# Optimization experiments

Hardware: AMD Instinct MI355X
Metric: run time of the kernel (lower is better)

Reference implementation:

```python
import jax, jax.numpy as jnp
import numpy as np

N_NODES = 100000
N_EDGES = 1600000
NUM_GRAPHS = 64
D = 128      # num_node_features
H = 256      # hidden_dim
OUT = 1      # output_dim
GA = 6       # num_graph_attributes


def setup_inputs() -> dict:
    key = jax.random.key(0)
    ks = jax.random.split(key, 20)
    p = lambda k, shape: (jax.random.normal(k, shape, jnp.float32) * 0.02)
    return {
        "x": jax.random.normal(ks[0], (N_NODES, D), jnp.float32),
        "edge_index": jax.random.randint(ks[1], (2, N_EDGES), 0, N_NODES),
        "batch": jnp.sort(jax.random.randint(ks[2], (N_NODES,), 0, NUM_GRAPHS)),
        "graph_attr": jax.random.normal(ks[3], (NUM_GRAPHS, GA), jnp.float32),
        # conv1 MLP: Linear(D->H), ReLU, Linear(H->H)
        "w1a": p(ks[4], (D, H)), "b1a": p(ks[5], (H,)),
        "w1b": p(ks[6], (H, H)), "b1b": p(ks[7], (H,)),
        # conv2 MLP: Linear(H->H), ReLU, Linear(H->H)
        "w2a": p(ks[8], (H, H)), "b2a": p(ks[9], (H,)),
        "w2b": p(ks[10], (H, H)), "b2b": p(ks[11], (H,)),
        # head
        "wf1": p(ks[12], (H + GA, H)), "bf1": p(ks[13], (H,)),
        "wf2": p(ks[14], (H, OUT)), "bf2": p(ks[15], (OUT,)),
    }


def _gin_conv(x, src, dst, wa, ba, wb, bb):
    # GINConv with default eps=0: MLP((1+0)*x_i + sum_{j->i} x_j)
    agg = jax.ops.segment_sum(x[src], dst, num_segments=N_NODES)  # [N, d]
    h = x + agg
    h = jax.nn.relu(h @ wa + ba)
    return h @ wb + bb


def reference(x, edge_index, batch, graph_attr,
              w1a, b1a, w1b, b1b, w2a, b2a, w2b, b2b,
              wf1, bf1, wf2, bf2):
    src, dst = edge_index[0], edge_index[1]
    h = jax.nn.relu(_gin_conv(x, src, dst, w1a, b1a, w1b, b1b))  # [N, H]
    h = _gin_conv(h, src, dst, w2a, b2a, w2b, b2b)               # [N, H]
    # global mean pool per graph
    sums = jax.ops.segment_sum(h, batch, num_segments=NUM_GRAPHS)          # [G, H]
    cnts = jax.ops.segment_sum(jnp.ones((h.shape[0], 1), h.dtype), batch,
                               num_segments=NUM_GRAPHS)                    # [G, 1]
    pooled = sums / jnp.maximum(cnts, 1.0)
    g = jnp.concatenate([pooled, graph_attr.reshape(-1, GA)], axis=1)      # [G, H+GA]
    g = jax.nn.relu(g @ wf1 + bf1)
    return g @ wf2 + bf2                                                   # [G, OUT]
```

## Files before the change

kernel.cpp:

```cpp
#include <hip/hip_runtime.h>

#define N_NODES 100000
#define N_EDGES 1600000
#define NGRAPH  64
#define DIN     128
#define HID     256
#define GA      6

#define NBUCK  98
#define BSHIFT 10
#define BCAP   20480

typedef __attribute__((ext_vector_type(8))) short bf16x8;
typedef __attribute__((ext_vector_type(4))) float f32x4;

__device__ __forceinline__ unsigned short f2bf(float f) {
  unsigned int u = __float_as_uint(f);
  u += 0x7fffu + ((u >> 16) & 1u);
  return (unsigned short)(u >> 16);
}
__device__ __forceinline__ float bf_lo(unsigned int u) { return __uint_as_float(u << 16); }
__device__ __forceinline__ float bf_hi(unsigned int u) { return __uint_as_float(u & 0xffff0000u); }
__device__ __forceinline__ unsigned int packbf(float lo, float hi) {
  return (unsigned int)f2bf(lo) | ((unsigned int)f2bf(hi) << 16);
}

__device__ __forceinline__ void gload16(const void* g, void* l) {
  __builtin_amdgcn_global_load_lds(
      (const __attribute__((address_space(1))) unsigned int*)g,
      (__attribute__((address_space(3))) unsigned int*)l, 16, 0, 0);
}


__global__ __launch_bounds__(256) void cvt_x_kernel(const float* __restrict__ in,
                                                    unsigned short* __restrict__ out) {
  size_t idx = ((size_t)blockIdx.x * 256 + threadIdx.x) * 4;
  float4 v = *(const float4*)&in[idx];
  ushort4 o;
  o.x = f2bf(v.x); o.y = f2bf(v.y); o.z = f2bf(v.z); o.w = f2bf(v.w);
  *(ushort4*)&out[idx] = o;
}

__global__ __launch_bounds__(256) void cvt_w_all(const float* __restrict__ w1a,
                                                 const float* __restrict__ w1b,
                                                 const float* __restrict__ w2a,
                                                 const float* __restrict__ w2b,
                                                 unsigned short* __restrict__ o1a,
                                                 unsigned short* __restrict__ o1b,
                                                 unsigned short* __restrict__ o2a,
                                                 unsigned short* __restrict__ o2b) {
  int bid = blockIdx.x, tid = threadIdx.x;
  const float* in; unsigned short* out; int shift, idx;
  if (bid < 128)      { in = w1a; out = o1a; shift = 7; idx = bid * 256 + tid; }
  else if (bid < 384) { in = w1b; out = o1b; shift = 8; idx = (bid - 128) * 256 + tid; }
  else if (bid < 640) { in = w2a; out = o2a; shift = 8; idx = (bid - 384) * 256 + tid; }
  else                { in = w2b; out = o2b; shift = 8; idx = (bid - 640) * 256 + tid; }
  int K = 1 << shift;
  int n = idx >> shift;
  int k = idx & (K - 1);
  out[idx] = f2bf(in[(size_t)k * HID + n]);
}


__global__ __launch_bounds__(256) void bin_kernel(const int* __restrict__ esrc,
                                                  const int* __restrict__ edst,
                                                  int* __restrict__ cursor,
                                                  unsigned int* __restrict__ tmp) {
  __shared__ unsigned int pk[4096];
  __shared__ int hist[NBUCK], lbase[NBUCK + 1], gbase[NBUCK], lcur[NBUCK];
  const int tid = threadIdx.x;
  const int lane = tid & 63;
  const int ebase = blockIdx.x * 4096;
  const int n = min(4096, N_EDGES - ebase);
  if (tid < NBUCK) hist[tid] = 0;
  __syncthreads();
  unsigned int pkv[16]; int bk[16];
#pragma unroll
  for (int i = 0; i < 16; i++) {
    int e = ebase + i * 256 + tid;
    bk[i] = -1;
    if (e < N_EDGES) {
      int s = esrc[e], d = edst[e];
      bk[i] = d >> BSHIFT;
      pkv[i] = (unsigned int)s | ((unsigned int)(d & ((1 << BSHIFT) - 1)) << 17);
      atomicAdd(&hist[bk[i]], 1);
    }
  }
  __syncthreads();
  if (tid < 64) {
    int i0 = 2 * tid, i1 = i0 + 1;
    int a0 = (i0 < NBUCK) ? hist[i0] : 0;
    int a1 = (i1 < NBUCK) ? hist[i1] : 0;
    int p = a0 + a1, sc = p;
#pragma unroll
    for (int off = 1; off < 64; off <<= 1) {
      int t = __shfl_up(sc, off);
      if (lane >= off) sc += t;
    }
    int excl = sc - p;
    if (i0 < NBUCK) lbase[i0] = excl;
    if (i1 < NBUCK) lbase[i1] = excl + a0;
    if (tid == 63) lbase[NBUCK] = sc;
  }
  __syncthreads();
  if (tid < NBUCK) {
    int c = hist[tid];
    gbase[tid] = c ? atomicAdd(&cursor[tid], c) : 0;
    lcur[tid] = lbase[tid];
  }
  __syncthreads();
#pragma unroll
  for (int i = 0; i < 16; i++) {
    if (bk[i] >= 0) {
      int pos = atomicAdd(&lcur[bk[i]], 1);
      pk[pos] = pkv[i];
    }
  }
  __syncthreads();
#pragma unroll
  for (int i = 0; i < 16; i++) {
    int idx = i * 256 + tid;
    if (idx < n) {
      int lo = 0, hi = NBUCK;
      while (hi - lo > 1) {
        int mid = (lo + hi) >> 1;
        if (lbase[mid] <= idx) lo = mid; else hi = mid;
      }
      tmp[(size_t)lo * BCAP + gbase[lo] + (idx - lbase[lo])] = pk[idx];
    }
  }
}


__global__ __launch_bounds__(512) void sort_kernel(const unsigned int* __restrict__ tmp,
                                                   const int* __restrict__ cnt,
                                                   int* __restrict__ csr,
                                                   int* __restrict__ ssrc) {
  __shared__ int nhist[1024], ncur[1024];
  __shared__ int bb[NBUCK];
  __shared__ int wsum[8];
  const int b = blockIdx.x;
  const int tid = threadIdx.x;
  const int lane = tid & 63, wid = tid >> 6;
  if (tid < 64) {
    int i0 = 2 * tid, i1 = i0 + 1;
    int a0 = (i0 < NBUCK) ? cnt[i0] : 0;
    int a1 = (i1 < NBUCK) ? cnt[i1] : 0;
    int p = a0 + a1, sc = p;
#pragma unroll
    for (int off = 1; off < 64; off <<= 1) {
      int t = __shfl_up(sc, off);
      if (lane >= off) sc += t;
    }
    int excl = sc - p;
    if (i0 < NBUCK) bb[i0] = excl;
    if (i1 < NBUCK) bb[i1] = excl + a0;
  }
  nhist[tid] = 0; nhist[tid + 512] = 0;
  __syncthreads();
  const int myCnt = cnt[b];
  const int ebase = bb[b];
  const unsigned int* srcp = tmp + (size_t)b * BCAP;
  for (int i = tid; i < myCnt; i += 512)
    atomicAdd(&nhist[srcp[i] >> 17], 1);
  __syncthreads();
  int i0 = 2 * tid;
  int a0 = nhist[i0], a1 = nhist[i0 + 1];
  int p = a0 + a1, sc = p;
#pragma unroll
  for (int off = 1; off < 64; off <<= 1) {
    int t = __shfl_up(sc, off);
    if (lane >= off) sc += t;
  }
  if (lane == 63) wsum[wid] = sc;
  __syncthreads();
  if (tid < 8) {
    int ws = wsum[tid];
#pragma unroll
    for (int off = 1; off < 8; off <<= 1) {
      int t = __shfl_up(ws, off);
      if (tid >= off) ws += t;
    }
    wsum[tid] = ws;
  }
  __syncthreads();
  int excl = ((wid > 0) ? wsum[wid - 1] : 0) + sc - p;
  ncur[i0] = excl;
  ncur[i0 + 1] = excl + a0;
  int node0 = (b << BSHIFT) + i0;
  if (node0 < N_NODES) csr[node0] = ebase + excl;
  if (node0 + 1 < N_NODES) csr[node0 + 1] = ebase + excl + a0;
  if (b == 0 && tid == 0) csr[N_NODES] = N_EDGES;
  __syncthreads();
  for (int i = tid; i < myCnt; i += 512) {
    unsigned int pe = srcp[i];
    int pos = atomicAdd(&ncur[pe >> 17], 1);
    ssrc[ebase + pos] = (int)(pe & 0x1FFFF);
  }
}


__global__ __launch_bounds__(256) void agg1_kernel(const unsigned int* __restrict__ x,
                                                   const int* __restrict__ csr,
                                                   const int* __restrict__ ssrc,
                                                   unsigned int* __restrict__ out) {
  int node = blockIdx.x * 4 + (threadIdx.x >> 6);
  int lane = threadIdx.x & 63;
  unsigned int u = x[(size_t)node * 64 + lane];
  float alo = bf_lo(u), ahi = bf_hi(u);
  int s = csr[node], e = csr[node + 1];
  int i = s;
  for (; i + 4 <= e; i += 4) {
    int n0 = ssrc[i], n1 = ssrc[i + 1], n2 = ssrc[i + 2], n3 = ssrc[i + 3];
    unsigned int v0 = x[(size_t)n0 * 64 + lane];
    unsigned int v1 = x[(size_t)n1 * 64 + lane];
    unsigned int v2 = x[(size_t)n2 * 64 + lane];
    unsigned int v3 = x[(size_t)n3 * 64 + lane];
    alo += bf_lo(v0) + bf_lo(v1) + bf_lo(v2) + bf_lo(v3);
    ahi += bf_hi(v0) + bf_hi(v1) + bf_hi(v2) + bf_hi(v3);
  }
  for (; i < e; i++) {
    unsigned int v = x[(size_t)ssrc[i] * 64 + lane];
    alo += bf_lo(v); ahi += bf_hi(v);
  }
  out[(size_t)node * 64 + lane] = packbf(alo, ahi);
}

__global__ __launch_bounds__(256) void agg2_kernel(const uint2* __restrict__ x,
                                                   const int* __restrict__ csr,
                                                   const int* __restrict__ ssrc,
                                                   uint2* __restrict__ out) {
  int node = blockIdx.x * 4 + (threadIdx.x >> 6);
  int lane = threadIdx.x & 63;
  uint2 u = x[(size_t)node * 64 + lane];
  float a0 = bf_lo(u.x), a1 = bf_hi(u.x), a2 = bf_lo(u.y), a3 = bf_hi(u.y);
  int s = csr[node], e = csr[node + 1];
  int i = s;
  for (; i + 4 <= e; i += 4) {
    int n0 = ssrc[i], n1 = ssrc[i + 1], n2 = ssrc[i + 2], n3 = ssrc[i + 3];
    uint2 v0 = x[(size_t)n0 * 64 + lane];
    uint2 v1 = x[(size_t)n1 * 64 + lane];
    uint2 v2 = x[(size_t)n2 * 64 + lane];
    uint2 v3 = x[(size_t)n3 * 64 + lane];
    a0 += bf_lo(v0.x) + bf_lo(v1.x) + bf_lo(v2.x) + bf_lo(v3.x);
    a1 += bf_hi(v0.x) + bf_hi(v1.x) + bf_hi(v2.x) + bf_hi(v3.x);
    a2 += bf_lo(v0.y) + bf_lo(v1.y) + bf_lo(v2.y) + bf_lo(v3.y);
    a3 += bf_hi(v0.y) + bf_hi(v1.y) + bf_hi(v2.y) + bf_hi(v3.y);
  }
  for (; i < e; i++) {
    uint2 v = x[(size_t)ssrc[i] * 64 + lane];
    a0 += bf_lo(v.x); a1 += bf_hi(v.x);
    a2 += bf_lo(v.y); a3 += bf_hi(v.y);
  }
  uint2 o;
  o.x = packbf(a0, a1);
  o.y = packbf(a2, a3);
  out[(size_t)node * 64 + lane] = o;
}

template<int K1, bool RELU2>
__global__ __launch_bounds__(512, 1)
void mlp_fused(const unsigned short* __restrict__ A,
               const unsigned short* __restrict__ W1t,
               const float* __restrict__ b1,
               const unsigned short* __restrict__ W2t,
               const float* __restrict__ b2,
               unsigned short* __restrict__ C) {
  __shared__ unsigned short Hsl[128 * 256];
  __shared__ unsigned short Wsl[2][256 * 64];
  unsigned short* const Ab0 = Hsl;
  unsigned short* const Ab1 = Hsl + 128 * 64;

  const int tid = threadIdx.x;
  const int lane = tid & 63;
  const int w = tid >> 6;
  const int wm = w >> 2;
  const int wn = w & 3;
  const int l15 = lane & 15, l4 = lane >> 4;
  const int l7 = l15 & 7;
  const int rowBase = blockIdx.x * 128;
  constexpr int S1 = K1 / 64;

  auto stageW = [&](const unsigned short* Wt, int K, int k0, unsigned short* dst) {
#pragma unroll
    for (int i = 0; i < 4; i++) {
      int c = i * 512 + tid;
      int n = c >> 3, koL = c & 7;
      int koS = koL ^ (n & 7);
      gload16(&Wt[(size_t)n * K + k0 + koS * 8], dst + (size_t)c * 8);
    }
  };
  auto stageA = [&](int k0, unsigned short* dst) {
#pragma unroll
    for (int i = 0; i < 2; i++) {
      int c = i * 512 + tid;
      int m = c >> 3, koL = c & 7;
      int koS = koL ^ (m & 7);
      int gr = rowBase + m; if (gr >= N_NODES) gr = N_NODES - 1;
      gload16(&A[(size_t)gr * K1 + k0 + koS * 8], dst + (size_t)c * 8);
    }
  };

  stageA(0, Ab0);
  stageW(W1t, K1, 0, Wsl[0]);
  __syncthreads();

  f32x4 acc[4][4] = {};

  for (int s = 0; s < S1; s++) {
    if (s + 1 < S1) {
      stageA((s + 1) * 64, ((s + 1) & 1) ? Ab1 : Ab0);
      stageW(W1t, K1, (s + 1) * 64, Wsl[(s + 1) & 1]);
    } else {
      stageW(W2t, 256, 0, Wsl[(s + 1) & 1]);
    }
    const unsigned short* Ac = (s & 1) ? Ab1 : Ab0;
    const unsigned short* Wc = Wsl[s & 1];
#pragma unroll
    for (int kk = 0; kk < 2; kk++) {
      int koX = (kk * 4 + l4) ^ l7;
      bf16x8 a[4], b[4];
#pragma unroll
      for (int f = 0; f < 4; f++) {
        int rowA = wm * 64 + f * 16 + l15;
        int rowB = wn * 64 + f * 16 + l15;
        a[f] = *(const bf16x8*)&Ac[(size_t)(rowA * 64 + koX * 8)];
        b[f] = *(const bf16x8*)&Wc[(size_t)(rowB * 64 + koX * 8)];
      }
#pragma unroll
      for (int fm = 0; fm < 4; fm++)
#pragma unroll
        for (int fn = 0; fn < 4; fn++)
          acc[fm][fn] = __builtin_amdgcn_mfma_f32_16x16x32_bf16(a[fm], b[fn], acc[fm][fn], 0, 0, 0);
    }
    __syncthreads();
  }

#pragma unroll
  for (int fm = 0; fm < 4; fm++) {
#pragma unroll
    for (int fn = 0; fn < 4; fn++) {
      int col = wn * 64 + fn * 16 + l15;
      float bb = b1[col];
#pragma unroll
      for (int j = 0; j < 4; j++) {
        int m = wm * 64 + fm * 16 + l4 * 4 + j;
        float v = fmaxf(acc[fm][fn][j] + bb, 0.f);
        float pv = __shfl_xor(v, 1);
        if ((l15 & 1) == 0) {
          int idx = m * 256 + (((col >> 3) ^ (m & 7)) << 3) + (col & 7);
          *(unsigned int*)&Hsl[idx] = packbf(v, pv);
        }
      }
      acc[fm][fn] = (f32x4){0.f, 0.f, 0.f, 0.f};
    }
  }
  __syncthreads();

  int wp = S1 & 1;
  for (int s2 = 0; s2 < 4; s2++) {
    if (s2 < 3) stageW(W2t, 256, (s2 + 1) * 64, Wsl[wp ^ 1]);
    const unsigned short* Wc = Wsl[wp];
#pragma unroll
    for (int kk = 0; kk < 2; kk++) {
      int ko = kk * 4 + l4;
      int koXw = ko ^ l7;
      int koXh = (s2 * 8 + ko) ^ l7;
      bf16x8 a[4], b[4];
#pragma unroll
      for (int f = 0; f < 4; f++) {
        int rowA = wm * 64 + f * 16 + l15;
        int rowB = wn * 64 + f * 16 + l15;
        a[f] = *(const bf16x8*)&Hsl[(size_t)(rowA * 256 + koXh * 8)];
        b[f] = *(const bf16x8*)&Wc[(size_t)(rowB * 64 + koXw * 8)];
      }
#pragma unroll
      for (int fm = 0; fm < 4; fm++)
#pragma unroll
        for (int fn = 0; fn < 4; fn++)
          acc[fm][fn] = __builtin_amdgcn_mfma_f32_16x16x32_bf16(a[fm], b[fn], acc[fm][fn], 0, 0, 0);
    }
    __syncthreads();
    wp ^= 1;
  }

#pragma unroll
  for (int fm = 0; fm < 4; fm++) {
    int r0 = rowBase + wm * 64 + fm * 16 + l4 * 4;
#pragma unroll
    for (int fn = 0; fn < 4; fn++) {
      int col = wn * 64 + fn * 16 + l15;
      float bb = b2[col];
#pragma unroll
      for (int j = 0; j < 4; j++) {
        int r = r0 + j;
        if (r < N_NODES) {
          float v = acc[fm][fn][j] + bb;
          if (RELU2) v = fmaxf(v, 0.f);
          C[(size_t)r * HID + col] = f2bf(v);
        }
      }
    }
  }
}


__global__ __launch_bounds__(256) void pool_kernel(const unsigned short* __restrict__ H,
                                                   const int* __restrict__ batch,
                                                   float* __restrict__ sums,
                                                   float* __restrict__ cnts) {
  int d = threadIdx.x;
  int n0 = blockIdx.x * 128;
  int n1 = n0 + 128; if (n1 > N_NODES) n1 = N_NODES;
  int cur = batch[n0];
  float run = 0.f, runc = 0.f;
  for (int i = n0; i < n1; i++) {
    int b = batch[i];
    if (b != cur) {
      atomicAdd(&sums[(size_t)cur * HID + d], run);
      if (d == 0) atomicAdd(&cnts[cur], runc);
      run = 0.f; runc = 0.f; cur = b;
    }
    run += __uint_as_float(((unsigned int)H[(size_t)i * HID + d]) << 16);
    runc += 1.f;
  }
  atomicAdd(&sums[(size_t)cur * HID + d], run);
  if (d == 0) atomicAdd(&cnts[cur], runc);
}


__global__ __launch_bounds__(256) void head_kernel(const float* __restrict__ sums,
                                                   const float* __restrict__ cnts,
                                                   const float* __restrict__ gattr,
                                                   const float* __restrict__ wf1,
                                                   const float* __restrict__ bf1,
                                                   const float* __restrict__ wf2,
                                                   const float* __restrict__ bf2,
                                                   float* __restrict__ out) {
  int g = blockIdx.x, tid = threadIdx.x;
  __shared__ float gv[HID + GA];
  __shared__ float red[256];
  float c = cnts[g]; c = fmaxf(c, 1.0f);
  gv[tid] = sums[(size_t)g * HID + tid] / c;
  if (tid < GA) gv[HID + tid] = gattr[g * GA + tid];
  __syncthreads();
  float acc = bf1[tid];
  for (int k = 0; k < HID + GA; k++)
    acc = fmaf(gv[k], wf1[(size_t)k * HID + tid], acc);
  float h = fmaxf(acc, 0.f);
  red[tid] = h * wf2[tid];
  __syncthreads();
  for (int s = 128; s > 0; s >>= 1) {
    if (tid < s) red[tid] += red[tid + s];
    __syncthreads();
  }
  if (tid == 0) out[g] = red[0] + bf2[0];
}


extern "C" void kernel_launch(void* const* d_in, const int* in_sizes, int n_in,
                              void* d_out, int out_size, void* d_ws, size_t ws_size,
                              hipStream_t stream) {
  const float* x     = (const float*)d_in[0];
  const int*   eidx  = (const int*)d_in[1];
  const int*   batch = (const int*)d_in[2];
  const float* gattr = (const float*)d_in[3];
  const float* w1a = (const float*)d_in[4];  const float* b1a = (const float*)d_in[5];
  const float* w1b = (const float*)d_in[6];  const float* b1b = (const float*)d_in[7];
  const float* w2a = (const float*)d_in[8];  const float* b2a = (const float*)d_in[9];
  const float* w2b = (const float*)d_in[10]; const float* b2b = (const float*)d_in[11];
  const float* wf1 = (const float*)d_in[12]; const float* bf1 = (const float*)d_in[13];
  const float* wf2 = (const float*)d_in[14]; const float* bf2 = (const float*)d_in[15];
  float* out = (float*)d_out;

  const int* esrc = eidx;
  const int* edst = eidx + N_EDGES;

  char* w = (char*)d_ws;
  auto alloc = [&](size_t bytes) -> void* {
    void* p = (void*)w;
    w += (bytes + 255) & ~(size_t)255;
    return p;
  };
  unsigned short* B0 = (unsigned short*)alloc((size_t)N_NODES * DIN * 2);
  unsigned short* B1 = (unsigned short*)alloc((size_t)N_NODES * HID * 2);
  unsigned short* B2 = (unsigned short*)alloc((size_t)N_NODES * HID * 2);
  unsigned short* w1aT = (unsigned short*)alloc(256 * 128 * 2);
  unsigned short* w1bT = (unsigned short*)alloc(256 * 256 * 2);
  unsigned short* w2aT = (unsigned short*)alloc(256 * 256 * 2);
  unsigned short* w2bT = (unsigned short*)alloc(256 * 256 * 2);
  int*   csr    = (int*)alloc((N_NODES + 4) * 4);
  int*   cursor = (int*)alloc(NBUCK * 4);
  unsigned int* tmp = (unsigned int*)alloc((size_t)NBUCK * BCAP * 4);
  int*   ssrc   = (int*)alloc((size_t)N_EDGES * 4);
  float* sums   = (float*)alloc((size_t)NGRAPH * HID * 4);
  float* cnts   = (float*)alloc(NGRAPH * 4);

  hipMemsetAsync(cursor, 0, NBUCK * 4, stream);
  hipMemsetAsync(sums, 0, (size_t)NGRAPH * HID * 4 + 256, stream);

  cvt_x_kernel<<<12500, 256, 0, stream>>>(x, B0);
  cvt_w_all<<<896, 256, 0, stream>>>(w1a, w1b, w2a, w2b, w1aT, w1bT, w2aT, w2bT);

  bin_kernel<<<(N_EDGES + 4095) / 4096, 256, 0, stream>>>(esrc, edst, cursor, tmp);
  sort_kernel<<<NBUCK, 512, 0, stream>>>(tmp, cursor, csr, ssrc);

  const int nconv = (N_NODES + 127) / 128;
  agg1_kernel<<<N_NODES / 4, 256, 0, stream>>>((const unsigned int*)B0, csr, ssrc,
                                               (unsigned int*)B1);
  mlp_fused<128, true><<<nconv, 512, 0, stream>>>(B1, w1aT, b1a, w1bT, b1b, B2);
  agg2_kernel<<<N_NODES / 4, 256, 0, stream>>>((const uint2*)B2, csr, ssrc, (uint2*)B1);
  mlp_fused<256, false><<<nconv, 512, 0, stream>>>(B1, w2aT, b2a, w2bT, b2b, B2);

  pool_kernel<<<(N_NODES + 127) / 128, 256, 0, stream>>>(B2, batch, sums, cnts);
  head_kernel<<<NGRAPH, 256, 0, stream>>>(sums, cnts, gattr, wf1, bf1, wf2, bf2, out);
}
```

Baseline: 478.2 us.

## Merge conversion kernels, store bucket ids in LDS, split aggregation launches in halves

Fuses the x and weight bf16 conversion kernels into a single launch so there is one fewer kernel boundary. In the binning kernel, each edge's bucket id is stored in a shared byte array so the scatter phase no longer does a binary search over bucket bases. The two aggregation kernels are each split into two launches over halves of the node range, which adds launches and gives no obvious benefit beyond possibly different scheduling.

```diff
diff --git a/kernel.cpp b/kernel.cpp
--- a/kernel.cpp
+++ b/kernel.cpp
@@ -32,24 +32,26 @@
 }
 
 
-__global__ __launch_bounds__(256) void cvt_x_kernel(const float* __restrict__ in,
-                                                    unsigned short* __restrict__ out) {
-  size_t idx = ((size_t)blockIdx.x * 256 + threadIdx.x) * 4;
-  float4 v = *(const float4*)&in[idx];
-  ushort4 o;
-  o.x = f2bf(v.x); o.y = f2bf(v.y); o.z = f2bf(v.z); o.w = f2bf(v.w);
-  *(ushort4*)&out[idx] = o;
-}
-
-__global__ __launch_bounds__(256) void cvt_w_all(const float* __restrict__ w1a,
-                                                 const float* __restrict__ w1b,
-                                                 const float* __restrict__ w2a,
-                                                 const float* __restrict__ w2b,
-                                                 unsigned short* __restrict__ o1a,
-                                                 unsigned short* __restrict__ o1b,
-                                                 unsigned short* __restrict__ o2a,
-                                                 unsigned short* __restrict__ o2b) {
+__global__ __launch_bounds__(256) void cvt_all(const float* __restrict__ x,
+                                               const float* __restrict__ w1a,
+                                               const float* __restrict__ w1b,
+                                               const float* __restrict__ w2a,
+                                               const float* __restrict__ w2b,
+                                               unsigned short* __restrict__ xo,
+                                               unsigned short* __restrict__ o1a,
+                                               unsigned short* __restrict__ o1b,
+                                               unsigned short* __restrict__ o2a,
+                                               unsigned short* __restrict__ o2b) {
   int bid = blockIdx.x, tid = threadIdx.x;
+  if (bid < 12500) {
+    size_t idx = ((size_t)bid * 256 + tid) * 4;
+    float4 v = *(const float4*)&x[idx];
+    ushort4 o;
+    o.x = f2bf(v.x); o.y = f2bf(v.y); o.z = f2bf(v.z); o.w = f2bf(v.w);
+    *(ushort4*)&xo[idx] = o;
+    return;
+  }
+  bid -= 12500;
   const float* in; unsigned short* out; int shift, idx;
   if (bid < 128)      { in = w1a; out = o1a; shift = 7; idx = bid * 256 + tid; }
   else if (bid < 384) { in = w1b; out = o1b; shift = 8; idx = (bid - 128) * 256 + tid; }
@@ -67,6 +69,7 @@
                                                   int* __restrict__ cursor,
                                                   unsigned int* __restrict__ tmp) {
   __shared__ unsigned int pk[4096];
+  __shared__ unsigned char bkb[4096];
   __shared__ int hist[NBUCK], lbase[NBUCK + 1], gbase[NBUCK], lcur[NBUCK];
   const int tid = threadIdx.x;
   const int lane = tid & 63;
@@ -114,6 +117,7 @@
     if (bk[i] >= 0) {
       int pos = atomicAdd(&lcur[bk[i]], 1);
       pk[pos] = pkv[i];
+      bkb[pos] = (unsigned char)bk[i];
     }
   }
   __syncthreads();
@@ -121,12 +125,8 @@
   for (int i = 0; i < 16; i++) {
     int idx = i * 256 + tid;
     if (idx < n) {
-      int lo = 0, hi = NBUCK;
-      while (hi - lo > 1) {
-        int mid = (lo + hi) >> 1;
-        if (lbase[mid] <= idx) lo = mid; else hi = mid;
-      }
-      tmp[(size_t)lo * BCAP + gbase[lo] + (idx - lbase[lo])] = pk[idx];
+      int b = bkb[idx];
+      tmp[(size_t)b * BCAP + gbase[b] + (idx - lbase[b])] = pk[idx];
     }
   }
 }
@@ -203,8 +203,9 @@
 __global__ __launch_bounds__(256) void agg1_kernel(const unsigned int* __restrict__ x,
                                                    const int* __restrict__ csr,
                                                    const int* __restrict__ ssrc,
-                                                   unsigned int* __restrict__ out) {
-  int node = blockIdx.x * 4 + (threadIdx.x >> 6);
+                                                   unsigned int* __restrict__ out,
+                                                   int base) {
+  int node = base + blockIdx.x * 4 + (threadIdx.x >> 6);
   int lane = threadIdx.x & 63;
   unsigned int u = x[(size_t)node * 64 + lane];
   float alo = bf_lo(u), ahi = bf_hi(u);
@@ -229,8 +230,9 @@
 __global__ __launch_bounds__(256) void agg2_kernel(const uint2* __restrict__ x,
                                                    const int* __restrict__ csr,
                                                    const int* __restrict__ ssrc,
-                                                   uint2* __restrict__ out) {
-  int node = blockIdx.x * 4 + (threadIdx.x >> 6);
+                                                   uint2* __restrict__ out,
+                                                   int base) {
+  int node = base + blockIdx.x * 4 + (threadIdx.x >> 6);
   int lane = threadIdx.x & 63;
   uint2 u = x[(size_t)node * 64 + lane];
   float a0 = bf_lo(u.x), a1 = bf_hi(u.x), a2 = bf_lo(u.y), a3 = bf_hi(u.y);
@@ -499,17 +501,21 @@
   hipMemsetAsync(cursor, 0, NBUCK * 4, stream);
   hipMemsetAsync(sums, 0, (size_t)NGRAPH * HID * 4 + 256, stream);
 
-  cvt_x_kernel<<<12500, 256, 0, stream>>>(x, B0);
-  cvt_w_all<<<896, 256, 0, stream>>>(w1a, w1b, w2a, w2b, w1aT, w1bT, w2aT, w2bT);
+  cvt_all<<<12500 + 896, 256, 0, stream>>>(x, w1a, w1b, w2a, w2b,
+                                           B0, w1aT, w1bT, w2aT, w2bT);
 
   bin_kernel<<<(N_EDGES + 4095) / 4096, 256, 0, stream>>>(esrc, edst, cursor, tmp);
   sort_kernel<<<NBUCK, 512, 0, stream>>>(tmp, cursor, csr, ssrc);
 
   const int nconv = (N_NODES + 127) / 128;
-  agg1_kernel<<<N_NODES / 4, 256, 0, stream>>>((const unsigned int*)B0, csr, ssrc,
-                                               (unsigned int*)B1);
+  const int half = N_NODES / 2;
+  agg1_kernel<<<half / 4, 256, 0, stream>>>((const unsigned int*)B0, csr, ssrc,
+                                            (unsigned int*)B1, 0);
+  agg1_kernel<<<half / 4, 256, 0, stream>>>((const unsigned int*)B0, csr, ssrc,
+                                            (unsigned int*)B1, half);
   mlp_fused<128, true><<<nconv, 512, 0, stream>>>(B1, w1aT, b1a, w1bT, b1b, B2);
-  agg2_kernel<<<N_NODES / 4, 256, 0, stream>>>((const uint2*)B2, csr, ssrc, (uint2*)B1);
+  agg2_kernel<<<half / 4, 256, 0, stream>>>((const uint2*)B2, csr, ssrc, (uint2*)B1, 0);
+  agg2_kernel<<<half / 4, 256, 0, stream>>>((const uint2*)B2, csr, ssrc, (uint2*)B1, half);
   mlp_fused<256, false><<<nconv, 512, 0, stream>>>(B1, w2aT, b2a, w2bT, b2b, B2);
 
   pool_kernel<<<(N_NODES + 127) / 128, 256, 0, stream>>>(B2, batch, sums, cnts);
```

Measured after the change: 483.3 us. Within noise of the previous version (+1.1%).
